# Optimization experiments

Measured on AMD Instinct MI355X. Metric: run time of the kernel, lower is better.

The kernel has to match this reference:

```python
import jax, jax.numpy as jnp
import numpy as np

B, E, N = 8, 256, 32          # triples, padded edges per triple, neighbors per edge
D, RD = 512, 768              # graph_dim, relation-semantic dim
R = 2000                      # num relations
L = 2                         # relation-context layers
K = 8                         # top_k neighbor similarity
M, HEADS = 32, 8              # memory tokens, memory-attention heads
HLLM = 4096                   # llm hidden size
EPS = 1e-5


def _ln(x, g, b):
    mu = jnp.mean(x, -1, keepdims=True)
    var = jnp.mean(jnp.square(x - mu), -1, keepdims=True)
    return (x - mu) * jax.lax.rsqrt(var + EPS) * g + b


def setup_inputs() -> dict:
    key = jax.random.key(0)
    ks = iter(jax.random.split(key, 40))
    nrm = lambda shape, s=0.02: jax.random.normal(next(ks), shape, jnp.float32) * s
    return {
        'edge_rel_ids': jax.random.randint(next(ks), (B, E), 0, R, jnp.int32),
        'neighbor_rel_ids': jax.random.randint(next(ks), (B, E, N), 0, R, jnp.int32),
        'edge_mask': jnp.ones((B, E), jnp.float32),
        'rel_emb': nrm((R, RD), 1.0),
        'rp_w': nrm((D, RD)), 'rp_b': jnp.zeros((D,), jnp.float32),
        'ly_vw': nrm((L, D, D)), 'ly_vb': jnp.zeros((L, D), jnp.float32),
        'ly_ow': nrm((L, D, D)), 'ly_ob': jnp.zeros((L, D), jnp.float32),
        'ly_n1g': jnp.ones((L, D), jnp.float32), 'ly_n1b': jnp.zeros((L, D), jnp.float32),
        'ly_n2g': jnp.ones((L, D), jnp.float32), 'ly_n2b': jnp.zeros((L, D), jnp.float32),
        'ly_w1': nrm((L, 4 * D, D)), 'ly_b1': jnp.zeros((L, 4 * D), jnp.float32),
        'ly_w2': nrm((L, D, 4 * D)), 'ly_b2': jnp.zeros((L, D), jnp.float32),
        'mem_q': nrm((M, D)),
        't_qw': nrm((D, D)), 't_qb': jnp.zeros((D,), jnp.float32),
        't_kw': nrm((D, D)), 't_kb': jnp.zeros((D,), jnp.float32),
        't_vw': nrm((D, D)), 't_vb': jnp.zeros((D,), jnp.float32),
        't_ow': nrm((D, D)), 't_ob': jnp.zeros((D,), jnp.float32),
        'proj_w': nrm((HLLM, D)), 'proj_b': jnp.zeros((HLLM,), jnp.float32),
    }


def reference(edge_rel_ids, neighbor_rel_ids, edge_mask, rel_emb, rp_w, rp_b,
              ly_vw, ly_vb, ly_ow, ly_ob, ly_n1g, ly_n1b, ly_n2g, ly_n2b,
              ly_w1, ly_b1, ly_w2, ly_b2, mem_q,
              t_qw, t_qb, t_kw, t_kb, t_vw, t_vb, t_ow, t_ob, proj_w, proj_b):
    rel_vector = lambda ids: rel_emb[ids] @ rp_w.T + rp_b  # embedding gather + rel_proj
    rel_vec = rel_vector(edge_rel_ids)            # [B,E,D]
    neigh = rel_vector(neighbor_rel_ids)          # [B,E,N,D] dominant gather traffic
    # per-edge cosine similarity to neighbor relations, top-k mean aggregation
    rn = rel_vec / jnp.maximum(jnp.linalg.norm(rel_vec, axis=-1, keepdims=True), 1e-12)
    nn_ = neigh / jnp.maximum(jnp.linalg.norm(neigh, axis=-1, keepdims=True), 1e-12)
    sims = jnp.einsum('bend,bed->ben', nn_, rn)   # [B,E,N]
    _, top_idx = jax.lax.top_k(sims, K)           # [B,E,K]
    agg = jnp.take_along_axis(neigh, top_idx[..., None], axis=2).mean(axis=2)  # [B,E,D]
    # RelationContextLayer stack. Each layer attends from one edge-state token to a
    # single context token: softmax over one key is identically 1, so the MHA
    # reduces exactly to out_proj(v_proj(context)) -- same math as torch MHA here.
    states = rel_vec
    for l in range(L):
        attn = (agg @ ly_vw[l].T + ly_vb[l]) @ ly_ow[l].T + ly_ob[l]
        states = _ln(states + attn, ly_n1g[l], ly_n1b[l])
        ff = jax.nn.gelu(states @ ly_w1[l].T + ly_b1[l], approximate=False) @ ly_w2[l].T + ly_b2[l]
        states = _ln(states + ff, ly_n2g[l], ly_n2b[l])
        states = states * edge_mask[..., None]
    # GraphMemoryTokenizer: learned queries cross-attend over padded edge states
    dh = D // HEADS
    q = (mem_q @ t_qw.T + t_qb).reshape(M, HEADS, dh)
    k = (states @ t_kw.T + t_kb).reshape(B, E, HEADS, dh)
    v = (states @ t_vw.T + t_vb).reshape(B, E, HEADS, dh)
    scores = jnp.einsum('mhd,behd->bhme', q, k) / jnp.sqrt(jnp.asarray(dh, q.dtype))
    scores = jnp.where(edge_mask[:, None, None, :] == 0, jnp.finfo(scores.dtype).min, scores)
    attnw = jax.nn.softmax(scores, axis=-1)
    mem = jnp.einsum('bhme,behd->bmhd', attnw, v).reshape(B, M, D)
    mem = mem @ t_ow.T + t_ob
    no_edges = jnp.sum(edge_mask, axis=1) == 0    # rows with zero edges -> zero memory
    mem = jnp.where(no_edges[:, None, None], 0.0, mem)
    return mem @ proj_w.T + proj_b                # [B,M,HLLM]
```

## Files before the change

kernel.cpp:

```cpp
#include <hip/hip_runtime.h>
#include <hip/hip_bf16.h>
#include <math.h>

#define B_   8
#define E_   256
#define N_   32
#define D_   512
#define RD_  768
#define R_   2000
#define L_   2
#define K_   8
#define M_   32
#define H_   8
#define DH_  64
#define HL_  4096

typedef float f32x4 __attribute__((ext_vector_type(4)));
typedef __bf16 bf16x8 __attribute__((ext_vector_type(8)));
typedef const __attribute__((address_space(1))) void GVoid;
typedef __attribute__((address_space(3))) void LVoid;

__device__ __forceinline__ float gelu_exact(float x) {
    return 0.5f * x * (1.0f + erff(x * 0.70710678118654752f));
}
__device__ __forceinline__ unsigned short f2bf(float x) {
    return __hip_bfloat16_raw(__float2bfloat16(x)).x;
}

template <int TM, int TN, int ACT_GELU, int OUT_BF16, int HAS_BIAS, int FLAGS>
__global__ __launch_bounds__(256) void gemm_mfma(const unsigned short* __restrict__ A,
                                                 const unsigned short* __restrict__ W,
                                                 const float* __restrict__ bias,
                                                 void* __restrict__ Cv,
                                                 int M, int N, int K,
                                                 size_t sA, size_t sW, size_t sC,
                                                 const float* __restrict__ rowflag) {
    constexpr int WTM = TM / 2, WTN = TN / 2;
    constexpr int RM = WTM / 16, RN = WTN / 16;
    constexpr int AI = TM / 32;
    constexpr int BI = TN / 32;
    __shared__ __align__(16) unsigned short As[TM * 64];
    __shared__ __align__(16) unsigned short Bs[TN * 64];

    const size_t z = blockIdx.z;
    A += z * sA; W += z * sW;

    const int tid = threadIdx.x;
    const int wave = tid >> 6, lane = tid & 63;
    const int quad = lane >> 4, l16 = lane & 15;
    const int wm = wave >> 1, wn = wave & 1;
    const int bm = blockIdx.y * TM, bn = blockIdx.x * TN;

    const int sub = lane >> 3;
    const int cpr = (lane & 7) ^ sub;

    f32x4 acc[RM][RN];
#pragma unroll
    for (int i = 0; i < RM; i++)
#pragma unroll
        for (int j = 0; j < RN; j++) acc[i][j] = (f32x4){0.f, 0.f, 0.f, 0.f};

    for (int k0 = 0; k0 < K; k0 += 64) {
        __syncthreads();
#pragma unroll
        for (int i = 0; i < AI; i++) {
            int r0 = (wave * AI + i) * 8;
            const unsigned short* g = A + (size_t)(bm + r0 + sub) * K + k0 + cpr * 8;
            __builtin_amdgcn_global_load_lds((GVoid*)g, (LVoid*)&As[r0 * 64], 16, 0, 0);
        }
#pragma unroll
        for (int i = 0; i < BI; i++) {
            int r0 = (wave * BI + i) * 8;
            const unsigned short* g = W + (size_t)(bn + r0 + sub) * K + k0 + cpr * 8;
            __builtin_amdgcn_global_load_lds((GVoid*)g, (LVoid*)&Bs[r0 * 64], 16, 0, 0);
        }
        __syncthreads();

#pragma unroll
        for (int h = 0; h < 2; h++) {
            bf16x8 af[RM], bf[RN];
#pragma unroll
            for (int i = 0; i < RM; i++) {
                int r = wm * WTM + i * 16 + l16;
                int ch = (h * 4 + quad) ^ (r & 7);
                af[i] = *(const bf16x8*)&As[r * 64 + ch * 8];
            }
#pragma unroll
            for (int j = 0; j < RN; j++) {
                int r = wn * WTN + j * 16 + l16;
                int ch = (h * 4 + quad) ^ (r & 7);
                bf[j] = *(const bf16x8*)&Bs[r * 64 + ch * 8];
            }
#pragma unroll
            for (int i = 0; i < RM; i++)
#pragma unroll
                for (int j = 0; j < RN; j++)
                    acc[i][j] = __builtin_amdgcn_mfma_f32_16x16x32_bf16(af[i], bf[j], acc[i][j], 0, 0, 0);
        }
    }

#pragma unroll
    for (int i = 0; i < RM; i++) {
#pragma unroll
        for (int j = 0; j < RN; j++) {
            int c = bn + wn * WTN + j * 16 + l16;
            float bv = HAS_BIAS ? bias[c] : 0.f;
#pragma unroll
            for (int reg = 0; reg < 4; reg++) {
                int r = bm + wm * WTM + i * 16 + quad * 4 + reg;
                if (r < M) {
                    float v = acc[i][j][reg] + bv;
                    if (ACT_GELU) v = gelu_exact(v);
                    if (FLAGS) v *= rowflag[r >> 5];
                    if (OUT_BF16)
                        ((unsigned short*)(Cv))[z * sC + (size_t)r * N + c] = f2bf(v);
                    else
                        ((float*)(Cv))[z * sC + (size_t)r * N + c] = v;
                }
            }
        }
    }
}

struct PrepArgs {
    const float* src[9];
    unsigned short* dst[9];
    int cum4[10];
    int nb_cvt, nb_tr, nb_bf, total4;
    const float* ly_vw; unsigned short* vwT;
    const float* ly_ow; const float* ly_vb; const float* ly_ob; float* bfuse;
    const float* t_kb; const float* t_vb; float* kvb;
    const float* edge_mask; float* flags;
    const float* mem_q; const float* t_qw; const float* t_qb; float* qbuf;
};

__global__ __launch_bounds__(256) void prep_all(PrepArgs a) {
    int bx = blockIdx.x, tid = threadIdx.x;
    if (bx < a.nb_cvt) {
        int i = bx * 256 + tid;
        if (i < a.total4) {
            int k = 0;
#pragma unroll
            for (int j = 0; j < 8; j++) if (i >= a.cum4[j + 1]) k = j + 1;
            int o = i - a.cum4[k];
            float4 v = ((const float4*)a.src[k])[o];
            ushort4 u;
            u.x = f2bf(v.x); u.y = f2bf(v.y); u.z = f2bf(v.z); u.w = f2bf(v.w);
            ((ushort4*)a.dst[k])[o] = u;
        }
        return;
    }
    bx -= a.nb_cvt;
    if (bx < a.nb_tr) {
        __shared__ float tile[32][33];
        int l = bx >> 8, t16 = bx & 255;
        int j0 = (t16 >> 4) * 32, k0 = (t16 & 15) * 32;
        int tx = tid & 31, ty = tid >> 5;
        const float* src = a.ly_vw + (size_t)l * 512 * 512;
        for (int r = ty; r < 32; r += 8)
            tile[r][tx] = src[(size_t)(j0 + r) * 512 + k0 + tx];
        __syncthreads();
        unsigned short* dst = a.vwT + (size_t)l * 512 * 512;
        for (int r = ty; r < 32; r += 8)
            dst[(size_t)(k0 + r) * 512 + j0 + tx] = f2bf(tile[tx][r]);
        return;
    }
    bx -= a.nb_tr;
    if (bx < a.nb_bf) {
        int wid = bx * 4 + (tid >> 6);
        int z = wid >> 9, n = wid & 511, lane = tid & 63;
        const float* owr = a.ly_ow + (size_t)z * 512 * 512 + (size_t)n * 512;
        const float* vbr = a.ly_vb + (size_t)z * 512;
        float s = 0.f;
#pragma unroll
        for (int j = 0; j < 8; j++) s += owr[lane + 64 * j] * vbr[lane + 64 * j];
#pragma unroll
        for (int off = 32; off; off >>= 1) s += __shfl_xor(s, off, 64);
        if (lane == 0) a.bfuse[z * 512 + n] = s + a.ly_ob[z * 512 + n];
        return;
    }
    bx -= a.nb_bf;
    if (bx < 1) {
        for (int n = tid; n < 512; n += 256) {
            a.kvb[n] = a.t_kb[n];
            a.kvb[n + 512] = a.t_vb[n];
        }
        __shared__ float red[4];
        for (int b = 0; b < B_; b++) {
            float s = a.edge_mask[b * E_ + tid];
#pragma unroll
            for (int off = 32; off; off >>= 1) s += __shfl_xor(s, off, 64);
            if ((tid & 63) == 0) red[tid >> 6] = s;
            __syncthreads();
            if (tid == 0)
                a.flags[b] = (red[0] + red[1] + red[2] + red[3] == 0.f) ? 0.f : 1.f;
            __syncthreads();
        }
        return;
    }
    bx -= 1;
    {
        int wid = bx * 4 + (tid >> 6);
        int m = wid >> 9, n = wid & 511, lane = tid & 63;
        const float* ar = a.mem_q + (size_t)m * 512;
        const float* br = a.t_qw + (size_t)n * 512;
        float s = 0.f;
#pragma unroll
        for (int j = 0; j < 8; j++) s += ar[lane + 64 * j] * br[lane + 64 * j];
#pragma unroll
        for (int off = 32; off; off >>= 1) s += __shfl_xor(s, off, 64);
        if (lane == 0) a.qbuf[(size_t)m * 512 + n] = s + a.t_qb[n];
    }
}

__global__ void sim_topk_agg(const int* __restrict__ eids, const int* __restrict__ nids,
                             const float* __restrict__ proj,
                             unsigned short* __restrict__ agg_bf, float* __restrict__ states) {
    int be = blockIdx.x, tid = threadIdx.x;
    __shared__ float ev[512];
    __shared__ float sims[32];
    __shared__ int nid_s[32];
    __shared__ int sel[8];

    int eid = eids[be];
    const float* ep = proj + (size_t)eid * D_;
    float e0 = ep[tid], e1 = ep[tid + 256];
    ev[tid] = e0; ev[tid + 256] = e1;
    states[(size_t)be * D_ + tid] = e0;
    states[(size_t)be * D_ + tid + 256] = e1;
    if (tid < 32) nid_s[tid] = nids[be * N_ + tid];
    __syncthreads();

    int wid = tid >> 6, lane = tid & 63;
    float se = 0.f;
#pragma unroll
    for (int j = 0; j < 8; j++) { float v = ev[lane + 64 * j]; se += v * v; }
#pragma unroll
    for (int off = 32; off; off >>= 1) se += __shfl_xor(se, off, 64);
    float en = fmaxf(sqrtf(se), 1e-12f);

    for (int n = wid; n < N_; n += 4) {
        int nid = nid_s[n];
        const float* np = proj + (size_t)nid * D_;
        float s = 0.f, s2 = 0.f;
#pragma unroll
        for (int j = 0; j < 8; j++) {
            float v = np[lane + 64 * j];
            s += v * ev[lane + 64 * j];
            s2 += v * v;
        }
#pragma unroll
        for (int off = 32; off; off >>= 1) {
            s += __shfl_xor(s, off, 64);
            s2 += __shfl_xor(s2, off, 64);
        }
        if (lane == 0) sims[n] = s / (fmaxf(sqrtf(s2), 1e-12f) * en);
    }
    __syncthreads();

    if (tid == 0) {
        unsigned used = 0;
        for (int k = 0; k < K_; k++) {
            float best = -3.402823466e38f; int bi = 0;
            for (int n = 0; n < N_; n++)
                if (!((used >> n) & 1u) && sims[n] > best) { best = sims[n]; bi = n; }
            used |= 1u << bi;
            sel[k] = nid_s[bi];
        }
    }
    __syncthreads();

    float a0 = 0.f, a1 = 0.f;
#pragma unroll
    for (int k = 0; k < K_; k++) {
        const float* sp = proj + (size_t)sel[k] * D_;
        a0 += sp[tid]; a1 += sp[tid + 256];
    }
    agg_bf[(size_t)be * D_ + tid] = f2bf(a0 * 0.125f);
    agg_bf[(size_t)be * D_ + tid + 256] = f2bf(a1 * 0.125f);
}

__global__ void add_ln_kernel(const float* __restrict__ x, const float* __restrict__ y,
                              int ystride, const float* __restrict__ g,
                              const float* __restrict__ bb, const float* __restrict__ mask,
                              float* __restrict__ out, unsigned short* __restrict__ out_bf) {
    int t = blockIdx.x, tid = threadIdx.x;
    const float* xr = x + (size_t)t * D_;
    const float* yr = y + (size_t)t * ystride;
    float x0 = xr[tid] + yr[tid];
    float x1 = xr[tid + 256] + yr[tid + 256];
    __shared__ float red[8];
    float s = x0 + x1;
#pragma unroll
    for (int off = 32; off; off >>= 1) s += __shfl_xor(s, off, 64);
    int wid = tid >> 6;
    if ((tid & 63) == 0) red[wid] = s;
    __syncthreads();
    float mean = (red[0] + red[1] + red[2] + red[3]) * (1.f / 512.f);
    float d0 = x0 - mean, d1 = x1 - mean;
    float v = d0 * d0 + d1 * d1;
#pragma unroll
    for (int off = 32; off; off >>= 1) v += __shfl_xor(v, off, 64);
    if ((tid & 63) == 0) red[4 + wid] = v;
    __syncthreads();
    float var = (red[4] + red[5] + red[6] + red[7]) * (1.f / 512.f);
    float rs = rsqrtf(var + 1e-5f);
    float mv = mask ? mask[t] : 1.f;
    float o0 = (d0 * rs * g[tid] + bb[tid]) * mv;
    float o1 = (d1 * rs * g[tid + 256] + bb[tid + 256]) * mv;
    out[(size_t)t * D_ + tid] = o0;
    out[(size_t)t * D_ + tid + 256] = o1;
    out_bf[(size_t)t * D_ + tid] = f2bf(o0);
    out_bf[(size_t)t * D_ + tid + 256] = f2bf(o1);
}

__global__ void mem_attn(const float* __restrict__ qb, const float* __restrict__ kv,
                         const float* __restrict__ mask, unsigned short* __restrict__ memb) {
    int idx = blockIdx.x;
    int b = idx & 7;
    int h = (idx >> 3) & 7;
    int m = idx >> 6;
    int tid = threadIdx.x;
    __shared__ float qh[64];
    __shared__ float sc[256];
    __shared__ float red[8];
    __shared__ float oacc[4][64];

    float mk = mask[b * E_ + tid];
    if (tid < 64) qh[tid] = qb[m * D_ + h * DH_ + tid];
    __syncthreads();
    const float* kr = kv + ((size_t)(b * E_ + tid)) * 1024 + h * DH_;
    float s = 0.f;
#pragma unroll
    for (int d = 0; d < DH_; d += 4) {
        float4 k4 = *(const float4*)(kr + d);
        s += k4.x * qh[d] + k4.y * qh[d + 1] + k4.z * qh[d + 2] + k4.w * qh[d + 3];
    }
    s *= 0.125f;
    if (mk == 0.f) s = -3.402823466e38f;
    float mx = s;
#pragma unroll
    for (int off = 32; off; off >>= 1) mx = fmaxf(mx, __shfl_xor(mx, off, 64));
    if ((tid & 63) == 0) red[tid >> 6] = mx;
    __syncthreads();
    mx = fmaxf(fmaxf(red[0], red[1]), fmaxf(red[2], red[3]));
    float p = expf(s - mx);
    float sum = p;
#pragma unroll
    for (int off = 32; off; off >>= 1) sum += __shfl_xor(sum, off, 64);
    if ((tid & 63) == 0) red[4 + (tid >> 6)] = sum;
    __syncthreads();
    sum = red[4] + red[5] + red[6] + red[7];
    sc[tid] = p / sum;
    __syncthreads();
    int d = tid & 63, part = tid >> 6;
    const float* vcol = kv + ((size_t)(b * E_ + part * 64)) * 1024 + 512 + h * DH_ + d;
    float acc = 0.f;
#pragma unroll 8
    for (int e = 0; e < 64; e++) acc += sc[part * 64 + e] * vcol[(size_t)e * 1024];
    oacc[part][d] = acc;
    __syncthreads();
    if (part == 0)
        memb[((size_t)(b * M_ + m)) * D_ + h * DH_ + d] =
            f2bf(oacc[0][d] + oacc[1][d] + oacc[2][d] + oacc[3][d]);
}

extern "C" void kernel_launch(void* const* d_in, const int* in_sizes, int n_in,
                              void* d_out, int out_size, void* d_ws, size_t ws_size,
                              hipStream_t stream) {
    const int*   edge_rel_ids     = (const int*)d_in[0];
    const int*   neighbor_rel_ids = (const int*)d_in[1];
    const float* edge_mask        = (const float*)d_in[2];
    const float* rel_emb          = (const float*)d_in[3];
    const float* rp_w             = (const float*)d_in[4];
    const float* rp_b             = (const float*)d_in[5];
    const float* ly_vw            = (const float*)d_in[6];
    const float* ly_vb            = (const float*)d_in[7];
    const float* ly_ow            = (const float*)d_in[8];
    const float* ly_ob            = (const float*)d_in[9];
    const float* ly_n1g           = (const float*)d_in[10];
    const float* ly_n1b           = (const float*)d_in[11];
    const float* ly_n2g           = (const float*)d_in[12];
    const float* ly_n2b           = (const float*)d_in[13];
    const float* ly_w1            = (const float*)d_in[14];
    const float* ly_b1            = (const float*)d_in[15];
    const float* ly_w2            = (const float*)d_in[16];
    const float* ly_b2            = (const float*)d_in[17];
    const float* mem_q            = (const float*)d_in[18];
    const float* t_qw             = (const float*)d_in[19];
    const float* t_qb             = (const float*)d_in[20];
    const float* t_kw             = (const float*)d_in[21];
    const float* t_kb             = (const float*)d_in[22];
    const float* t_vw             = (const float*)d_in[23];
    const float* t_vb             = (const float*)d_in[24];
    const float* t_ow             = (const float*)d_in[25];
    const float* t_ob             = (const float*)d_in[26];
    const float* proj_w           = (const float*)d_in[27];
    const float* proj_b           = (const float*)d_in[28];
    float* out = (float*)d_out;
    (void)ws_size; (void)in_sizes; (void)n_in; (void)out_size;

    char* ws = (char*)d_ws;
    size_t off = 0;
    auto allocf = [&](size_t n) { float* p = (float*)(ws + off); off += ((n * 4 + 255) & ~(size_t)255); return p; };
    auto allocb = [&](size_t n) { unsigned short* p = (unsigned short*)(ws + off); off += ((n * 2 + 255) & ~(size_t)255); return p; };

    const int T = B_ * E_;

    float* proj    = allocf((size_t)R_ * D_);
    float* states  = allocf((size_t)T * D_);
    float* tmpB    = allocf((size_t)T * D_);
    float* attnall = allocf((size_t)T * 2 * D_);
    float* qbuf    = allocf((size_t)M_ * D_);
    float* bfuse   = allocf(2 * D_);
    float* kvb     = allocf(2 * D_);
    float* flags   = allocf(B_);
    float* kvbuf   = attnall;

    unsigned short* rel_bf    = allocb((size_t)2048 * RD_);
    unsigned short* rpw_bf    = allocb((size_t)D_ * RD_);
    unsigned short* agg_bf    = allocb((size_t)T * D_);
    unsigned short* states_bf = allocb((size_t)T * D_);
    unsigned short* ff1_bf    = allocb((size_t)T * 4 * D_);
    unsigned short* vwT_bf    = allocb((size_t)L_ * D_ * D_);
    unsigned short* ow_bf     = allocb((size_t)L_ * D_ * D_);
    unsigned short* wfuse_bf  = allocb((size_t)L_ * D_ * D_);
    unsigned short* w1_bf     = allocb((size_t)L_ * 4 * D_ * D_);
    unsigned short* w2_bf     = allocb((size_t)L_ * 4 * D_ * D_);
    unsigned short* kvw_bf    = allocb((size_t)2 * D_ * D_);
    unsigned short* tow_bf    = allocb((size_t)D_ * D_);
    unsigned short* pw_bf     = allocb((size_t)HL_ * D_);
    unsigned short* memb_bf   = allocb((size_t)B_ * M_ * D_);
    unsigned short* mem2_bf   = allocb((size_t)B_ * M_ * D_);

    PrepArgs a;
    int sizes[9] = { R_ * RD_, D_ * RD_, L_ * D_ * D_, L_ * 4 * D_ * D_,
                     L_ * 4 * D_ * D_, D_ * D_, D_ * D_, D_ * D_, HL_ * D_ };
    const float* srcs[9] = { rel_emb, rp_w, ly_ow, ly_w1, ly_w2, t_kw, t_vw, t_ow, proj_w };
    unsigned short* dsts[9] = { rel_bf, rpw_bf, ow_bf, w1_bf, w2_bf,
                                kvw_bf, kvw_bf + (size_t)D_ * D_, tow_bf, pw_bf };
    int cum = 0;
    for (int i = 0; i < 9; i++) {
        a.src[i] = srcs[i]; a.dst[i] = dsts[i];
        a.cum4[i] = cum; cum += sizes[i] / 4;
    }
    a.cum4[9] = cum;
    a.total4 = cum;
    a.nb_cvt = (cum + 255) / 256;
    a.nb_tr = 512;
    a.nb_bf = 256;
    a.ly_vw = ly_vw; a.vwT = vwT_bf;
    a.ly_ow = ly_ow; a.ly_vb = ly_vb; a.ly_ob = ly_ob; a.bfuse = bfuse;
    a.t_kb = t_kb; a.t_vb = t_vb; a.kvb = kvb;
    a.edge_mask = edge_mask; a.flags = flags;
    a.mem_q = mem_q; a.t_qw = t_qw; a.t_qb = t_qb; a.qbuf = qbuf;
    int nblk = a.nb_cvt + a.nb_tr + a.nb_bf + 1 + 4096;
    prep_all<<<nblk, 256, 0, stream>>>(a);

    gemm_mfma<32, 64, 0, 0, 1, 0><<<dim3(D_ / 64, 64), 256, 0, stream>>>(
        rel_bf, rpw_bf, rp_b, proj, R_, D_, RD_, 0, 0, 0, nullptr);
    sim_topk_agg<<<T, 256, 0, stream>>>(edge_rel_ids, neighbor_rel_ids, proj,
                                        agg_bf, states);

    gemm_mfma<32, 64, 0, 1, 0, 0><<<dim3(8, 16, 2), 256, 0, stream>>>(
        ow_bf, vwT_bf, nullptr, wfuse_bf, D_, D_, D_,
        (size_t)D_ * D_, (size_t)D_ * D_, (size_t)D_ * D_, nullptr);
    gemm_mfma<64, 64, 0, 0, 1, 0><<<dim3(2 * D_ / 64, T / 64), 256, 0, stream>>>(
        agg_bf, wfuse_bf, bfuse, attnall, T, 2 * D_, D_, 0, 0, 0, nullptr);

    for (int l = 0; l < L_; l++) {
        add_ln_kernel<<<T, 256, 0, stream>>>(states, attnall + (size_t)l * D_, 2 * D_,
                                             ly_n1g + l * D_, ly_n1b + l * D_, nullptr,
                                             states, states_bf);
        gemm_mfma<64, 64, 1, 1, 1, 0><<<dim3(4 * D_ / 64, T / 64), 256, 0, stream>>>(
            states_bf, w1_bf + (size_t)l * 4 * D_ * D_, ly_b1 + l * 4 * D_,
            ff1_bf, T, 4 * D_, D_, 0, 0, 0, nullptr);
        gemm_mfma<32, 64, 0, 0, 1, 0><<<dim3(D_ / 64, T / 32), 256, 0, stream>>>(
            ff1_bf, w2_bf + (size_t)l * 4 * D_ * D_, ly_b2 + l * D_,
            tmpB, T, D_, 4 * D_, 0, 0, 0, nullptr);
        add_ln_kernel<<<T, 256, 0, stream>>>(states, tmpB, D_,
                                             ly_n2g + l * D_, ly_n2b + l * D_, edge_mask,
                                             states, states_bf);
    }

    gemm_mfma<64, 64, 0, 0, 1, 0><<<dim3(2 * D_ / 64, T / 64), 256, 0, stream>>>(
        states_bf, kvw_bf, kvb, kvbuf, T, 2 * D_, D_, 0, 0, 0, nullptr);

    mem_attn<<<B_ * M_ * H_, 256, 0, stream>>>(qbuf, kvbuf, edge_mask, memb_bf);

    gemm_mfma<32, 64, 0, 1, 1, 1><<<dim3(D_ / 64, 8), 256, 0, stream>>>(
        memb_bf, tow_bf, t_ob, mem2_bf, B_ * M_, D_, D_, 0, 0, 0, flags);

    gemm_mfma<32, 64, 0, 0, 1, 0><<<dim3(HL_ / 64, 8), 256, 0, stream>>>(
        mem2_bf, pw_bf, proj_b, out, B_ * M_, HL_, D_, 0, 0, 0, nullptr);
}
```

Measured before the change: 322.1 us.

## Fuse add+LayerNorm into following GEMM prologues and merge independent GEMM launches

Removes the standalone add_ln kernels by computing residual-add LayerNorm statistics inside a new gemm_ln kernel, which normalizes rows while staging the A tile into LDS. Layer boundaries chain two LayerNorms (end of one layer, start of the next) in one prologue, and the final LN is folded into the K/V projection. The rel projection GEMM and the fused-weight GEMM now run in a single launch. Top-k selection moves from a serial single-thread loop to a wave-wide shuffle argmax. Each N-tile block recomputes the LN statistics and re-reads fp32 activations, trading redundant loads for fewer launches and intermediate round trips.

```diff
diff --git a/kernel.cpp b/kernel.cpp
--- a/kernel.cpp
+++ b/kernel.cpp
@@ -33,24 +33,18 @@
                                                  const float* __restrict__ bias,
                                                  void* __restrict__ Cv,
                                                  int M, int N, int K,
-                                                 size_t sA, size_t sW, size_t sC,
                                                  const float* __restrict__ rowflag) {
     constexpr int WTM = TM / 2, WTN = TN / 2;
     constexpr int RM = WTM / 16, RN = WTN / 16;
-    constexpr int AI = TM / 32;
-    constexpr int BI = TN / 32;
+    constexpr int AI = TM / 32, BI = TN / 32;
     __shared__ __align__(16) unsigned short As[TM * 64];
     __shared__ __align__(16) unsigned short Bs[TN * 64];
-
-    const size_t z = blockIdx.z;
-    A += z * sA; W += z * sW;
 
     const int tid = threadIdx.x;
     const int wave = tid >> 6, lane = tid & 63;
     const int quad = lane >> 4, l16 = lane & 15;
     const int wm = wave >> 1, wn = wave & 1;
     const int bm = blockIdx.y * TM, bn = blockIdx.x * TN;
-
     const int sub = lane >> 3;
     const int cpr = (lane & 7) ^ sub;
 
@@ -75,7 +69,6 @@
             __builtin_amdgcn_global_load_lds((GVoid*)g, (LVoid*)&Bs[r0 * 64], 16, 0, 0);
         }
         __syncthreads();
-
 #pragma unroll
         for (int h = 0; h < 2; h++) {
             bf16x8 af[RM], bf[RN];
@@ -113,10 +106,262 @@
                     if (ACT_GELU) v = gelu_exact(v);
                     if (FLAGS) v *= rowflag[r >> 5];
                     if (OUT_BF16)
-                        ((unsigned short*)(Cv))[z * sC + (size_t)r * N + c] = f2bf(v);
+                        ((unsigned short*)Cv)[(size_t)r * N + c] = f2bf(v);
                     else
-                        ((float*)(Cv))[z * sC + (size_t)r * N + c] = v;
+                        ((float*)Cv)[(size_t)r * N + c] = v;
                 }
+            }
+        }
+    }
+}
+
+__global__ __launch_bounds__(256) void projwfuse_kernel(
+        const unsigned short* __restrict__ rel_bf, const unsigned short* __restrict__ rpw_bf,
+        const float* __restrict__ rp_b, float* __restrict__ proj,
+        const unsigned short* __restrict__ ow_bf, const unsigned short* __restrict__ vwT_bf,
+        unsigned short* __restrict__ wfuse) {
+    __shared__ __align__(16) unsigned short As[32 * 64];
+    __shared__ __align__(16) unsigned short Bs[64 * 64];
+
+    const unsigned short *A, *W;
+    const float* bias;
+    int Mg, Kg, bm, bn, obf;
+    void* C;
+    int t = blockIdx.x;
+    if (t < 504) {
+        A = rel_bf; W = rpw_bf; bias = rp_b; Mg = R_; Kg = RD_;
+        C = proj; obf = 0; bn = (t & 7) * 64; bm = (t >> 3) * 32;
+    } else {
+        int u = t - 504, z = u >> 7, uu = u & 127;
+        A = ow_bf + (size_t)z * 262144; W = vwT_bf + (size_t)z * 262144;
+        bias = nullptr; Mg = 512; Kg = 512;
+        C = wfuse + (size_t)z * 262144; obf = 1; bn = (uu & 7) * 64; bm = (uu >> 3) * 32;
+    }
+
+    const int tid = threadIdx.x;
+    const int wave = tid >> 6, lane = tid & 63;
+    const int quad = lane >> 4, l16 = lane & 15;
+    const int wm = wave >> 1, wn = wave & 1;
+    const int sub = lane >> 3;
+    const int cpr = (lane & 7) ^ sub;
+
+    f32x4 acc[1][2];
+    acc[0][0] = (f32x4){0.f, 0.f, 0.f, 0.f};
+    acc[0][1] = (f32x4){0.f, 0.f, 0.f, 0.f};
+
+    for (int k0 = 0; k0 < Kg; k0 += 64) {
+        __syncthreads();
+        {
+            int r0 = wave * 8;
+            const unsigned short* g = A + (size_t)(bm + r0 + sub) * Kg + k0 + cpr * 8;
+            __builtin_amdgcn_global_load_lds((GVoid*)g, (LVoid*)&As[r0 * 64], 16, 0, 0);
+        }
+#pragma unroll
+        for (int i = 0; i < 2; i++) {
+            int r0 = (wave * 2 + i) * 8;
+            const unsigned short* g = W + (size_t)(bn + r0 + sub) * Kg + k0 + cpr * 8;
+            __builtin_amdgcn_global_load_lds((GVoid*)g, (LVoid*)&Bs[r0 * 64], 16, 0, 0);
+        }
+        __syncthreads();
+#pragma unroll
+        for (int h = 0; h < 2; h++) {
+            bf16x8 af, bf[2];
+            {
+                int r = wm * 16 + l16;
+                int ch = (h * 4 + quad) ^ (r & 7);
+                af = *(const bf16x8*)&As[r * 64 + ch * 8];
+            }
+#pragma unroll
+            for (int j = 0; j < 2; j++) {
+                int r = wn * 32 + j * 16 + l16;
+                int ch = (h * 4 + quad) ^ (r & 7);
+                bf[j] = *(const bf16x8*)&Bs[r * 64 + ch * 8];
+            }
+#pragma unroll
+            for (int j = 0; j < 2; j++)
+                acc[0][j] = __builtin_amdgcn_mfma_f32_16x16x32_bf16(af, bf[j], acc[0][j], 0, 0, 0);
+        }
+    }
+
+#pragma unroll
+    for (int j = 0; j < 2; j++) {
+        int c = bn + wn * 32 + j * 16 + l16;
+        float bv = bias ? bias[c] : 0.f;
+#pragma unroll
+        for (int reg = 0; reg < 4; reg++) {
+            int r = bm + wm * 16 + quad * 4 + reg;
+            if (r < Mg) {
+                float v = acc[0][j][reg] + bv;
+                if (obf)
+                    ((unsigned short*)C)[(size_t)r * 512 + c] = f2bf(v);
+                else
+                    ((float*)C)[(size_t)r * 512 + c] = v;
+            }
+        }
+    }
+}
+
+template <int ACT_GELU, int OUT_BF16, int LNMODE>
+__global__ __launch_bounds__(256) void gemm_ln(
+        const float* __restrict__ x, const float* __restrict__ y, int ystride,
+        const float* __restrict__ g1, const float* __restrict__ b1,
+        const float* __restrict__ mask1,
+        const float* __restrict__ y2, int y2stride,
+        const float* __restrict__ g2, const float* __restrict__ b2,
+        const unsigned short* __restrict__ W, const float* __restrict__ bias,
+        void* __restrict__ Cv, float* __restrict__ states_out, int N, int K) {
+    __shared__ __align__(16) unsigned short As[64 * 64];
+    __shared__ __align__(16) unsigned short Bs[64 * 64];
+    __shared__ float stats[5 * 64];
+    float* meanA = stats;
+    float* rsA = stats + 64;
+    float* mvA = stats + 128;
+    float* mean2A = stats + 192;
+    float* rs2A = stats + 256;
+
+    const int tid = threadIdx.x;
+    const int wave = tid >> 6, lane = tid & 63;
+    const int quad = lane >> 4, l16 = lane & 15;
+    const int wm = wave >> 1, wn = wave & 1;
+    const int bm = blockIdx.y * 64, bn = blockIdx.x * 64;
+    const int sub = lane >> 3;
+    const int cpr = (lane & 7) ^ sub;
+
+    for (int pass = 0; pass < 16; pass++) {
+        int i = pass * 4 + wave;
+        int r = bm + i;
+        const float* xr = x + (size_t)r * D_;
+        const float* yr = y + (size_t)r * ystride;
+        float vreg[8];
+        float s = 0.f;
+#pragma unroll
+        for (int j = 0; j < 8; j++) {
+            float v = xr[lane + 64 * j] + yr[lane + 64 * j];
+            vreg[j] = v; s += v;
+        }
+#pragma unroll
+        for (int off = 32; off; off >>= 1) s += __shfl_xor(s, off, 64);
+        float mean = s * (1.f / 512.f);
+        float var = 0.f;
+#pragma unroll
+        for (int j = 0; j < 8; j++) { float d = vreg[j] - mean; var += d * d; }
+#pragma unroll
+        for (int off = 32; off; off >>= 1) var += __shfl_xor(var, off, 64);
+        float rs = rsqrtf(var * (1.f / 512.f) + 1e-5f);
+        float mv = mask1 ? mask1[r] : 1.f;
+        if (LNMODE == 2) {
+            const float* y2r = y2 + (size_t)r * y2stride;
+            float treg[8];
+            float s2 = 0.f;
+#pragma unroll
+            for (int j = 0; j < 8; j++) {
+                int idx = lane + 64 * j;
+                float tv = ((vreg[j] - mean) * rs * g1[idx] + b1[idx]) * mv + y2r[idx];
+                treg[j] = tv; s2 += tv;
+            }
+#pragma unroll
+            for (int off = 32; off; off >>= 1) s2 += __shfl_xor(s2, off, 64);
+            float mean2 = s2 * (1.f / 512.f);
+            float var2 = 0.f;
+#pragma unroll
+            for (int j = 0; j < 8; j++) { float d = treg[j] - mean2; var2 += d * d; }
+#pragma unroll
+            for (int off = 32; off; off >>= 1) var2 += __shfl_xor(var2, off, 64);
+            float rs2 = rsqrtf(var2 * (1.f / 512.f) + 1e-5f);
+            if (lane == 0) {
+                meanA[i] = mean; rsA[i] = rs; mvA[i] = mv;
+                mean2A[i] = mean2; rs2A[i] = rs2;
+            }
+        } else {
+            if (lane == 0) { meanA[i] = mean; rsA[i] = rs; mvA[i] = mv; }
+        }
+    }
+
+    f32x4 acc[2][2];
+#pragma unroll
+    for (int i = 0; i < 2; i++)
+#pragma unroll
+        for (int j = 0; j < 2; j++) acc[i][j] = (f32x4){0.f, 0.f, 0.f, 0.f};
+
+    const bool wout = (states_out != nullptr) && (blockIdx.x == 0);
+
+    for (int k0 = 0; k0 < K; k0 += 64) {
+        __syncthreads();
+#pragma unroll
+        for (int i = 0; i < 2; i++) {
+            int r0 = (wave * 2 + i) * 8;
+            const unsigned short* g = W + (size_t)(bn + r0 + sub) * K + k0 + cpr * 8;
+            __builtin_amdgcn_global_load_lds((GVoid*)g, (LVoid*)&Bs[r0 * 64], 16, 0, 0);
+        }
+#pragma unroll
+        for (int rep = 0; rep < 2; rep++) {
+            int linear = tid + rep * 256;
+            int r = linear >> 3, c = linear & 7, slot = c ^ (r & 7);
+            int rg = bm + r, kg = k0 + c * 8;
+            const float* xr = x + (size_t)rg * D_ + kg;
+            const float* yr = y + (size_t)rg * ystride + kg;
+            float mean = meanA[r], rs = rsA[r], mv = mvA[r];
+            float outv[8];
+#pragma unroll
+            for (int j = 0; j < 8; j++) {
+                float v = ((xr[j] + yr[j]) - mean) * rs * g1[kg + j] + b1[kg + j];
+                v *= mv;
+                if (LNMODE == 2) {
+                    v = (v + y2[(size_t)rg * y2stride + kg + j] - mean2A[r]) * rs2A[r]
+                            * g2[kg + j] + b2[kg + j];
+                }
+                outv[j] = v;
+            }
+            if (wout) {
+#pragma unroll
+                for (int j = 0; j < 8; j++) states_out[(size_t)rg * D_ + kg + j] = outv[j];
+            }
+            uint4 pk;
+            pk.x = (unsigned)f2bf(outv[0]) | ((unsigned)f2bf(outv[1]) << 16);
+            pk.y = (unsigned)f2bf(outv[2]) | ((unsigned)f2bf(outv[3]) << 16);
+            pk.z = (unsigned)f2bf(outv[4]) | ((unsigned)f2bf(outv[5]) << 16);
+            pk.w = (unsigned)f2bf(outv[6]) | ((unsigned)f2bf(outv[7]) << 16);
+            *(uint4*)&As[r * 64 + slot * 8] = pk;
+        }
+        __syncthreads();
+#pragma unroll
+        for (int h = 0; h < 2; h++) {
+            bf16x8 af[2], bfv[2];
+#pragma unroll
+            for (int i = 0; i < 2; i++) {
+                int r = wm * 32 + i * 16 + l16;
+                int ch = (h * 4 + quad) ^ (r & 7);
+                af[i] = *(const bf16x8*)&As[r * 64 + ch * 8];
+            }
+#pragma unroll
+            for (int j = 0; j < 2; j++) {
+                int r = wn * 32 + j * 16 + l16;
+                int ch = (h * 4 + quad) ^ (r & 7);
+                bfv[j] = *(const bf16x8*)&Bs[r * 64 + ch * 8];
+            }
+#pragma unroll
+            for (int i = 0; i < 2; i++)
+#pragma unroll
+                for (int j = 0; j < 2; j++)
+                    acc[i][j] = __builtin_amdgcn_mfma_f32_16x16x32_bf16(af[i], bfv[j], acc[i][j], 0, 0, 0);
+        }
+    }
+
+#pragma unroll
+    for (int i = 0; i < 2; i++) {
+#pragma unroll
+        for (int j = 0; j < 2; j++) {
+            int c = bn + wn * 32 + j * 16 + l16;
+            float bv = bias[c];
+#pragma unroll
+            for (int reg = 0; reg < 4; reg++) {
+                int r = bm + wm * 32 + i * 16 + quad * 4 + reg;
+                float v = acc[i][j][reg] + bv;
+                if (ACT_GELU) v = gelu_exact(v);
+                if (OUT_BF16)
+                    ((unsigned short*)Cv)[(size_t)r * N + c] = f2bf(v);
+                else
+                    ((float*)Cv)[(size_t)r * N + c] = v;
             }
         }
     }
@@ -126,7 +371,7 @@
     const float* src[9];
     unsigned short* dst[9];
     int cum4[10];
-    int nb_cvt, nb_tr, nb_bf, total4;
+    int nb_cvt, total4;
     const float* ly_vw; unsigned short* vwT;
     const float* ly_ow; const float* ly_vb; const float* ly_ob; float* bfuse;
     const float* t_kb; const float* t_vb; float* kvb;
@@ -151,7 +396,7 @@
         return;
     }
     bx -= a.nb_cvt;
-    if (bx < a.nb_tr) {
+    if (bx < 512) {
         __shared__ float tile[32][33];
         int l = bx >> 8, t16 = bx & 255;
         int j0 = (t16 >> 4) * 32, k0 = (t16 & 15) * 32;
@@ -165,8 +410,8 @@
             dst[(size_t)(k0 + r) * 512 + j0 + tx] = f2bf(tile[tx][r]);
         return;
     }
-    bx -= a.nb_tr;
-    if (bx < a.nb_bf) {
+    bx -= 512;
+    if (bx < 256) {
         int wid = bx * 4 + (tid >> 6);
         int z = wid >> 9, n = wid & 511, lane = tid & 63;
         const float* owr = a.ly_ow + (size_t)z * 512 * 512 + (size_t)n * 512;
@@ -179,13 +424,13 @@
         if (lane == 0) a.bfuse[z * 512 + n] = s + a.ly_ob[z * 512 + n];
         return;
     }
-    bx -= a.nb_bf;
+    bx -= 256;
     if (bx < 1) {
+        __shared__ float red[4];
         for (int n = tid; n < 512; n += 256) {
             a.kvb[n] = a.t_kb[n];
             a.kvb[n + 512] = a.t_vb[n];
         }
-        __shared__ float red[4];
         for (int b = 0; b < B_; b++) {
             float s = a.edge_mask[b * E_ + tid];
 #pragma unroll
@@ -258,14 +503,19 @@
     }
     __syncthreads();
 
-    if (tid == 0) {
-        unsigned used = 0;
+    if (tid < 64) {
+        float v = (tid < 32) ? sims[tid] : -3.402823466e38f;
+        int idx = tid;
         for (int k = 0; k < K_; k++) {
-            float best = -3.402823466e38f; int bi = 0;
-            for (int n = 0; n < N_; n++)
-                if (!((used >> n) & 1u) && sims[n] > best) { best = sims[n]; bi = n; }
-            used |= 1u << bi;
-            sel[k] = nid_s[bi];
+            float bv = v; int bi = idx;
+#pragma unroll
+            for (int off = 32; off; off >>= 1) {
+                float ov = __shfl_xor(bv, off, 64);
+                int oi = __shfl_xor(bi, off, 64);
+                if (ov > bv || (ov == bv && oi < bi)) { bv = ov; bi = oi; }
+            }
+            if (tid == 0) sel[k] = nid_s[bi];
+            if (idx == bi) v = -3.402823466e38f;
         }
     }
     __syncthreads();
@@ -278,40 +528,6 @@
     }
     agg_bf[(size_t)be * D_ + tid] = f2bf(a0 * 0.125f);
     agg_bf[(size_t)be * D_ + tid + 256] = f2bf(a1 * 0.125f);
-}
-
-__global__ void add_ln_kernel(const float* __restrict__ x, const float* __restrict__ y,
-                              int ystride, const float* __restrict__ g,
-                              const float* __restrict__ bb, const float* __restrict__ mask,
-                              float* __restrict__ out, unsigned short* __restrict__ out_bf) {
-    int t = blockIdx.x, tid = threadIdx.x;
-    const float* xr = x + (size_t)t * D_;
-    const float* yr = y + (size_t)t * ystride;
-    float x0 = xr[tid] + yr[tid];
-    float x1 = xr[tid + 256] + yr[tid + 256];
-    __shared__ float red[8];
-    float s = x0 + x1;
-#pragma unroll
-    for (int off = 32; off; off >>= 1) s += __shfl_xor(s, off, 64);
-    int wid = tid >> 6;
-    if ((tid & 63) == 0) red[wid] = s;
-    __syncthreads();
-    float mean = (red[0] + red[1] + red[2] + red[3]) * (1.f / 512.f);
-    float d0 = x0 - mean, d1 = x1 - mean;
-    float v = d0 * d0 + d1 * d1;
-#pragma unroll
-    for (int off = 32; off; off >>= 1) v += __shfl_xor(v, off, 64);
-    if ((tid & 63) == 0) red[4 + wid] = v;
-    __syncthreads();
-    float var = (red[4] + red[5] + red[6] + red[7]) * (1.f / 512.f);
-    float rs = rsqrtf(var + 1e-5f);
-    float mv = mask ? mask[t] : 1.f;
-    float o0 = (d0 * rs * g[tid] + bb[tid]) * mv;
-    float o1 = (d1 * rs * g[tid + 256] + bb[tid + 256]) * mv;
-    out[(size_t)t * D_ + tid] = o0;
-    out[(size_t)t * D_ + tid + 256] = o1;
-    out_bf[(size_t)t * D_ + tid] = f2bf(o0);
-    out_bf[(size_t)t * D_ + tid + 256] = f2bf(o1);
 }
 
 __global__ void mem_attn(const float* __restrict__ qb, const float* __restrict__ kv,
@@ -409,6 +625,7 @@
 
     float* proj    = allocf((size_t)R_ * D_);
     float* states  = allocf((size_t)T * D_);
+    float* statesX = allocf((size_t)T * D_);
     float* tmpB    = allocf((size_t)T * D_);
     float* attnall = allocf((size_t)T * 2 * D_);
     float* qbuf    = allocf((size_t)M_ * D_);
@@ -417,21 +634,20 @@
     float* flags   = allocf(B_);
     float* kvbuf   = attnall;
 
-    unsigned short* rel_bf    = allocb((size_t)2048 * RD_);
-    unsigned short* rpw_bf    = allocb((size_t)D_ * RD_);
-    unsigned short* agg_bf    = allocb((size_t)T * D_);
-    unsigned short* states_bf = allocb((size_t)T * D_);
-    unsigned short* ff1_bf    = allocb((size_t)T * 4 * D_);
-    unsigned short* vwT_bf    = allocb((size_t)L_ * D_ * D_);
-    unsigned short* ow_bf     = allocb((size_t)L_ * D_ * D_);
-    unsigned short* wfuse_bf  = allocb((size_t)L_ * D_ * D_);
-    unsigned short* w1_bf     = allocb((size_t)L_ * 4 * D_ * D_);
-    unsigned short* w2_bf     = allocb((size_t)L_ * 4 * D_ * D_);
-    unsigned short* kvw_bf    = allocb((size_t)2 * D_ * D_);
-    unsigned short* tow_bf    = allocb((size_t)D_ * D_);
-    unsigned short* pw_bf     = allocb((size_t)HL_ * D_);
-    unsigned short* memb_bf   = allocb((size_t)B_ * M_ * D_);
-    unsigned short* mem2_bf   = allocb((size_t)B_ * M_ * D_);
+    unsigned short* rel_bf  = allocb((size_t)2048 * RD_);
+    unsigned short* rpw_bf  = allocb((size_t)D_ * RD_);
+    unsigned short* agg_bf  = allocb((size_t)T * D_);
+    unsigned short* ff1_bf  = allocb((size_t)T * 4 * D_);
+    unsigned short* vwT_bf  = allocb((size_t)L_ * D_ * D_);
+    unsigned short* ow_bf   = allocb((size_t)L_ * D_ * D_);
+    unsigned short* wfuse   = allocb((size_t)L_ * D_ * D_);
+    unsigned short* w1_bf   = allocb((size_t)L_ * 4 * D_ * D_);
+    unsigned short* w2_bf   = allocb((size_t)L_ * 4 * D_ * D_);
+    unsigned short* kvw_bf  = allocb((size_t)2 * D_ * D_);
+    unsigned short* tow_bf  = allocb((size_t)D_ * D_);
+    unsigned short* pw_bf   = allocb((size_t)HL_ * D_);
+    unsigned short* memb_bf = allocb((size_t)B_ * M_ * D_);
+    unsigned short* mem2_bf = allocb((size_t)B_ * M_ * D_);
 
     PrepArgs a;
     int sizes[9] = { R_ * RD_, D_ * RD_, L_ * D_ * D_, L_ * 4 * D_ * D_,
@@ -447,50 +663,46 @@
     a.cum4[9] = cum;
     a.total4 = cum;
     a.nb_cvt = (cum + 255) / 256;
-    a.nb_tr = 512;
-    a.nb_bf = 256;
     a.ly_vw = ly_vw; a.vwT = vwT_bf;
     a.ly_ow = ly_ow; a.ly_vb = ly_vb; a.ly_ob = ly_ob; a.bfuse = bfuse;
     a.t_kb = t_kb; a.t_vb = t_vb; a.kvb = kvb;
     a.edge_mask = edge_mask; a.flags = flags;
     a.mem_q = mem_q; a.t_qw = t_qw; a.t_qb = t_qb; a.qbuf = qbuf;
-    int nblk = a.nb_cvt + a.nb_tr + a.nb_bf + 1 + 4096;
+    int nblk = a.nb_cvt + 512 + 256 + 1 + 4096;
     prep_all<<<nblk, 256, 0, stream>>>(a);
 
-    gemm_mfma<32, 64, 0, 0, 1, 0><<<dim3(D_ / 64, 64), 256, 0, stream>>>(
-        rel_bf, rpw_bf, rp_b, proj, R_, D_, RD_, 0, 0, 0, nullptr);
+    projwfuse_kernel<<<760, 256, 0, stream>>>(rel_bf, rpw_bf, rp_b, proj,
+                                              ow_bf, vwT_bf, wfuse);
+
     sim_topk_agg<<<T, 256, 0, stream>>>(edge_rel_ids, neighbor_rel_ids, proj,
                                         agg_bf, states);
 
-    gemm_mfma<32, 64, 0, 1, 0, 0><<<dim3(8, 16, 2), 256, 0, stream>>>(
-        ow_bf, vwT_bf, nullptr, wfuse_bf, D_, D_, D_,
-        (size_t)D_ * D_, (size_t)D_ * D_, (size_t)D_ * D_, nullptr);
-    gemm_mfma<64, 64, 0, 0, 1, 0><<<dim3(2 * D_ / 64, T / 64), 256, 0, stream>>>(
-        agg_bf, wfuse_bf, bfuse, attnall, T, 2 * D_, D_, 0, 0, 0, nullptr);
-
-    for (int l = 0; l < L_; l++) {
-        add_ln_kernel<<<T, 256, 0, stream>>>(states, attnall + (size_t)l * D_, 2 * D_,
-                                             ly_n1g + l * D_, ly_n1b + l * D_, nullptr,
-                                             states, states_bf);
-        gemm_mfma<64, 64, 1, 1, 1, 0><<<dim3(4 * D_ / 64, T / 64), 256, 0, stream>>>(
-            states_bf, w1_bf + (size_t)l * 4 * D_ * D_, ly_b1 + l * 4 * D_,
-            ff1_bf, T, 4 * D_, D_, 0, 0, 0, nullptr);
-        gemm_mfma<32, 64, 0, 0, 1, 0><<<dim3(D_ / 64, T / 32), 256, 0, stream>>>(
-            ff1_bf, w2_bf + (size_t)l * 4 * D_ * D_, ly_b2 + l * D_,
-            tmpB, T, D_, 4 * D_, 0, 0, 0, nullptr);
-        add_ln_kernel<<<T, 256, 0, stream>>>(states, tmpB, D_,
-                                             ly_n2g + l * D_, ly_n2b + l * D_, edge_mask,
-                                             states, states_bf);
-    }
-
-    gemm_mfma<64, 64, 0, 0, 1, 0><<<dim3(2 * D_ / 64, T / 64), 256, 0, stream>>>(
-        states_bf, kvw_bf, kvb, kvbuf, T, 2 * D_, D_, 0, 0, 0, nullptr);
+    gemm_mfma<64, 64, 0, 0, 1, 0><<<dim3(16, 32), 256, 0, stream>>>(
+        agg_bf, wfuse, bfuse, attnall, T, 2 * D_, D_, nullptr);
+
+    gemm_ln<1, 1, 1><<<dim3(32, 32), 256, 0, stream>>>(
+        states, attnall, 2 * D_, ly_n1g, ly_n1b, nullptr,
+        nullptr, 0, nullptr, nullptr,
+        w1_bf, ly_b1, ff1_bf, statesX, 4 * D_, D_);
+    gemm_mfma<32, 64, 0, 0, 1, 0><<<dim3(8, 64), 256, 0, stream>>>(
+        ff1_bf, w2_bf, ly_b2, tmpB, T, D_, 4 * D_, nullptr);
+    gemm_ln<1, 1, 2><<<dim3(32, 32), 256, 0, stream>>>(
+        statesX, tmpB, D_, ly_n2g, ly_n2b, edge_mask,
+        attnall + D_, 2 * D_, ly_n1g + D_, ly_n1b + D_,
+        w1_bf + (size_t)4 * D_ * D_, ly_b1 + 4 * D_, ff1_bf, states, 4 * D_, D_);
+    gemm_mfma<32, 64, 0, 0, 1, 0><<<dim3(8, 64), 256, 0, stream>>>(
+        ff1_bf, w2_bf + (size_t)4 * D_ * D_, ly_b2 + D_, tmpB, T, D_, 4 * D_, nullptr);
+
+    gemm_ln<0, 0, 1><<<dim3(16, 32), 256, 0, stream>>>(
+        states, tmpB, D_, ly_n2g + D_, ly_n2b + D_, edge_mask,
+        nullptr, 0, nullptr, nullptr,
+        kvw_bf, kvb, kvbuf, nullptr, 2 * D_, D_);
 
     mem_attn<<<B_ * M_ * H_, 256, 0, stream>>>(qbuf, kvbuf, edge_mask, memb_bf);
 
-    gemm_mfma<32, 64, 0, 1, 1, 1><<<dim3(D_ / 64, 8), 256, 0, stream>>>(
-        memb_bf, tow_bf, t_ob, mem2_bf, B_ * M_, D_, D_, 0, 0, 0, flags);
-
-    gemm_mfma<32, 64, 0, 0, 1, 0><<<dim3(HL_ / 64, 8), 256, 0, stream>>>(
-        mem2_bf, pw_bf, proj_b, out, B_ * M_, HL_, D_, 0, 0, 0, nullptr);
-}
+    gemm_mfma<32, 64, 0, 1, 1, 1><<<dim3(8, 8), 256, 0, stream>>>(
+        memb_bf, tow_bf, t_ob, mem2_bf, B_ * M_, D_, D_, flags);
+
+    gemm_mfma<32, 64, 0, 0, 1, 0><<<dim3(64, 8), 256, 0, stream>>>(
+        mem2_bf, pw_bf, proj_b, out, B_ * M_, HL_, D_, nullptr);
+}
```

New measurement: 407.9 us. +26.7%, slower.
